# Optimization experiments

Hardware: AMD Instinct MI355X
Metric: run time of the kernel (lower is better)

## Reference

```python
import jax, jax.numpy as jnp
import numpy as np

B, T_RED, C = 16, 512, 512
MAX_DUR = 16


def setup_inputs() -> dict:
    key = jax.random.key(0)
    rng = np.random.default_rng(0)
    durs = np.zeros((B, T_RED), dtype=np.int32)
    for b in range(B):
        nv = int(rng.integers(T_RED // 2, T_RED + 1))
        durs[b, :nv] = rng.integers(1, MAX_DUR + 1, size=nv)
    target_T = durs.sum(axis=1).astype(np.int32)
    pooled_x = jax.random.normal(key, (B, T_RED, C), dtype=jnp.float32)
    return {
        "pooled_x": pooled_x,
        "durations": jnp.asarray(durs),
        "target_T": jnp.asarray(target_T),
    }


def reference(pooled_x, durations, target_T):
    # pooled_x: [B, T_red, C]; durations: [B, T_red] int (0 = pad); target_T: [B]
    Bv, T_red, Cv = pooled_x.shape
    max_len = int(jnp.max(target_T))  # concrete (eager) like the torch .item()

    # torch: valid_durs = durations[b][durations[b] > 0]; feats = pooled_x[b, :num_valid]
    # -> stably compact nonzero durations to the front; pair with leading features.
    order = jnp.argsort(jnp.where(durations > 0, 0, 1), axis=1, stable=True)
    d = jnp.take_along_axis(durations, order, axis=1)            # [B, T_red]
    csum = jnp.cumsum(d, axis=1)                                 # [B, T_red]

    t = jnp.arange(max_len, dtype=csum.dtype)                    # [max_len]
    # repeat_interleave inverse: output frame t belongs to segment
    # s = searchsorted(csum, t, 'right')  (csum[s-1] <= t < csum[s])
    seg = jax.vmap(lambda c: jnp.searchsorted(c, t, side="right"))(csum)  # [B, max_len]
    seg = jnp.minimum(seg, T_red - 1)

    total = csum[:, -1]                                          # len(repeat_interleave result)
    curr_len = jnp.minimum(total, target_T)                      # [B]
    valid = t[None, :] < curr_len[:, None]                       # [B, max_len]

    gathered = jnp.take_along_axis(pooled_x, seg[:, :, None], axis=1)  # [B, max_len, C]
    x_restored = jnp.where(valid[:, :, None], gathered, jnp.zeros((), pooled_x.dtype))
    new_mask = jnp.where(valid, 0, 1).astype(jnp.int32)          # 0 = valid, 1 = padded
    return x_restored, new_mask
```

## Files before the change

### kernel.cpp

```cpp
#include <hip/hip_runtime.h>
#include <hip/hip_bf16.h>

#define B_DIM 16
#define T_RED 512
#define C_DIM 512
#define ROWS_PER_BLK 16

typedef float vfloat4 __attribute__((ext_vector_type(4)));

__device__ inline int wave_incl_scan(int v) {
    #pragma unroll
    for (int off = 1; off < 64; off <<= 1) {
        int n = __shfl_up(v, off, 64);
        if ((threadIdx.x & 63) >= off) v += n;
    }
    return v;
}

__device__ inline int block_incl_scan(int v, int* wsum ) {
    const int lane = threadIdx.x & 63;
    const int wid  = threadIdx.x >> 6;
    int s = wave_incl_scan(v);
    if (lane == 63) wsum[wid] = s;
    __syncthreads();
    if (wid == 0 && lane < 8) {
        int w = wsum[lane];
        #pragma unroll
        for (int off = 1; off < 8; off <<= 1) {
            int n = __shfl_up(w, off, 8);
            if (lane >= off) w += n;
        }
        wsum[lane] = w;
    }
    __syncthreads();
    if (wid > 0) s += wsum[wid - 1];
    return s;
}

__global__ void build_rowmap(const int* __restrict__ durations,
                             int* __restrict__ rowsrc, int max_len) {
    const int b = blockIdx.x;
    const int tid = threadIdx.x;

    __shared__ int wsum[8];
    __shared__ int dcomp[T_RED];
    __shared__ int csum_s[T_RED];

    const int d = durations[b * T_RED + tid];
    const int f = (d > 0) ? 1 : 0;

    const int pos = block_incl_scan(f, wsum);
    dcomp[tid] = 0;
    __syncthreads();
    if (f) dcomp[pos - 1] = d;
    __syncthreads();

    const int myd = dcomp[tid];
    __syncthreads();
    const int cs = block_incl_scan(myd, wsum);
    csum_s[tid] = cs;
    __syncthreads();

    const int total = csum_s[T_RED - 1];
    const int start = cs - myd;
    const int srcrow = b * T_RED + tid;

    for (int k = 0; k < myd; ++k)
        rowsrc[b * max_len + start + k] = srcrow;

    for (int t = total + tid; t < max_len; t += T_RED)
        rowsrc[b * max_len + t] = -1;
}

__global__ __launch_bounds__(256) void scatter_rows(
        const vfloat4* __restrict__ x4,
        const int* __restrict__ rowsrc,
        vfloat4* __restrict__ out4,
        float* __restrict__ out_mask,
        int nrows) {
    __shared__ int ls[ROWS_PER_BLK];
    const int base = blockIdx.x * ROWS_PER_BLK;
    const int tid  = threadIdx.x;

    if (tid < ROWS_PER_BLK) {
        const int r = base + tid;
        const int s = (r < nrows) ? rowsrc[r] : -1;
        ls[tid] = s;
        if (r < nrows)
            __builtin_nontemporal_store((s >= 0) ? 0.0f : 1.0f, &out_mask[r]);
    }
    __syncthreads();

    const int c4   = tid & 127;
    const int half = tid >> 7;

    #pragma unroll
    for (int p = 0; p < 8; ++p) {
        const int lr = 2 * p + half;
        const int r  = base + lr;
        if (r < nrows) {
            const int s = ls[lr];
            vfloat4 v = (vfloat4)(0.0f);
            if (s >= 0) v = x4[(size_t)s * (C_DIM / 4) + c4];
            __builtin_nontemporal_store(v, &out4[(size_t)r * (C_DIM / 4) + c4]);
        }
    }
}

extern "C" void kernel_launch(void* const* d_in, const int* in_sizes, int n_in,
                              void* d_out, int out_size, void* d_ws, size_t ws_size,
                              hipStream_t stream) {
    const float* pooled_x  = (const float*)d_in[0];
    const int*   durations = (const int*)d_in[1];

    const int max_len = out_size / (B_DIM * (C_DIM + 1));
    const int nrows   = B_DIM * max_len;

    float* out_x    = (float*)d_out;
    float* out_mask = out_x + (size_t)nrows * C_DIM;

    int* rowsrc = (int*)d_ws;

    build_rowmap<<<B_DIM, T_RED, 0, stream>>>(durations, rowsrc, max_len);

    scatter_rows<<<(nrows + ROWS_PER_BLK - 1) / ROWS_PER_BLK, 256, 0, stream>>>(
        (const vfloat4*)pooled_x, rowsrc, (vfloat4*)out_x, out_mask, nrows);
}
```

Measured before the change: 161.7 us.

## Fuse row-map construction into scatter kernel with per-block scan and binary search

Removes the separate build_rowmap kernel and its global rowsrc buffer. Every scatter block now reloads its batch's durations, recomputes the compaction and cumulative sum in shared memory, and finds each output row's source segment by binary search. This drops one kernel launch and the serialized per-batch write loop, but repeats the scan work in every block. That adds several barriers before the copy phase starts.

```diff
diff --git a/kernel.cpp b/kernel.cpp
--- a/kernel.cpp
+++ b/kernel.cpp
@@ -8,101 +8,96 @@
 
 typedef float vfloat4 __attribute__((ext_vector_type(4)));
 
-__device__ inline int wave_incl_scan(int v) {
+__device__ inline int block_scan256(int v, int* wsum ) {
+    const int lane = threadIdx.x & 63;
+    const int wid  = threadIdx.x >> 6;
+    int s = v;
     #pragma unroll
     for (int off = 1; off < 64; off <<= 1) {
-        int n = __shfl_up(v, off, 64);
-        if ((threadIdx.x & 63) >= off) v += n;
+        int n = __shfl_up(s, off, 64);
+        if (lane >= off) s += n;
     }
-    return v;
+    if (lane == 63) wsum[wid] = s;
+    __syncthreads();
+    int add = 0;
+    #pragma unroll
+    for (int w = 0; w < 4; ++w)
+        if (w < wid) add += wsum[w];
+    int out = s + add;
+    __syncthreads();
+    return out;
 }
 
-__device__ inline int block_incl_scan(int v, int* wsum ) {
-    const int lane = threadIdx.x & 63;
-    const int wid  = threadIdx.x >> 6;
-    int s = wave_incl_scan(v);
-    if (lane == 63) wsum[wid] = s;
-    __syncthreads();
-    if (wid == 0 && lane < 8) {
-        int w = wsum[lane];
-        #pragma unroll
-        for (int off = 1; off < 8; off <<= 1) {
-            int n = __shfl_up(w, off, 8);
-            if (lane >= off) w += n;
-        }
-        wsum[lane] = w;
-    }
-    __syncthreads();
-    if (wid > 0) s += wsum[wid - 1];
-    return s;
-}
-
-__global__ void build_rowmap(const int* __restrict__ durations,
-                             int* __restrict__ rowsrc, int max_len) {
-    const int b = blockIdx.x;
-    const int tid = threadIdx.x;
-
-    __shared__ int wsum[8];
-    __shared__ int dcomp[T_RED];
-    __shared__ int csum_s[T_RED];
-
-    const int d = durations[b * T_RED + tid];
-    const int f = (d > 0) ? 1 : 0;
-
-    const int pos = block_incl_scan(f, wsum);
-    dcomp[tid] = 0;
-    __syncthreads();
-    if (f) dcomp[pos - 1] = d;
-    __syncthreads();
-
-    const int myd = dcomp[tid];
-    __syncthreads();
-    const int cs = block_incl_scan(myd, wsum);
-    csum_s[tid] = cs;
-    __syncthreads();
-
-    const int total = csum_s[T_RED - 1];
-    const int start = cs - myd;
-    const int srcrow = b * T_RED + tid;
-
-    for (int k = 0; k < myd; ++k)
-        rowsrc[b * max_len + start + k] = srcrow;
-
-    for (int t = total + tid; t < max_len; t += T_RED)
-        rowsrc[b * max_len + t] = -1;
-}
-
-__global__ __launch_bounds__(256) void scatter_rows(
+__global__ __launch_bounds__(256) void scatter_fused(
         const vfloat4* __restrict__ x4,
-        const int* __restrict__ rowsrc,
+        const int2* __restrict__ dur2,
         vfloat4* __restrict__ out4,
         float* __restrict__ out_mask,
-        int nrows) {
-    __shared__ int ls[ROWS_PER_BLK];
+        int max_len) {
+    const int b    = blockIdx.y;
     const int base = blockIdx.x * ROWS_PER_BLK;
     const int tid  = threadIdx.x;
 
+    __shared__ int dcomp[T_RED];
+    __shared__ int csum[T_RED];
+    __shared__ int wsum[4];
+    __shared__ int ls[ROWS_PER_BLK];
+
+    const int2 dd = dur2[b * (T_RED / 2) + tid];
+    const int d0 = dd.x, d1 = dd.y;
+    const int f0 = (d0 > 0) ? 1 : 0;
+    const int f1 = (d1 > 0) ? 1 : 0;
+
+    const int S1 = block_scan256(f0 + f1, wsum);
+    const int excl = S1 - f0 - f1;
+    dcomp[2 * tid]     = 0;
+    dcomp[2 * tid + 1] = 0;
+    __syncthreads();
+    if (f0) dcomp[excl] = d0;
+    if (f1) dcomp[excl + f0] = d1;
+    __syncthreads();
+
+    const int c0 = dcomp[2 * tid];
+    const int c1 = dcomp[2 * tid + 1];
+    const int S2 = block_scan256(c0 + c1, wsum);
+    csum[2 * tid]     = S2 - c1;
+    csum[2 * tid + 1] = S2;
+    __syncthreads();
+
+    const int total = csum[T_RED - 1];
+
     if (tid < ROWS_PER_BLK) {
-        const int r = base + tid;
-        const int s = (r < nrows) ? rowsrc[r] : -1;
-        ls[tid] = s;
-        if (r < nrows)
-            __builtin_nontemporal_store((s >= 0) ? 0.0f : 1.0f, &out_mask[r]);
+        const int t = base + tid;
+        int src = -1;
+        if (t < max_len && t < total) {
+            int idx = 0;
+            #pragma unroll
+            for (int w = 256; w >= 1; w >>= 1) {
+                const int cand = idx + w;
+                if (cand <= T_RED && csum[cand - 1] <= t) idx = cand;
+            }
+            const int seg = (idx < T_RED - 1) ? idx : (T_RED - 1);
+            src = b * T_RED + seg;
+        }
+        if (t < max_len) {
+            ls[tid] = src;
+            out_mask[(size_t)b * max_len + t] = (src >= 0) ? 0.0f : 1.0f;
+        }
     }
     __syncthreads();
 
     const int c4   = tid & 127;
     const int half = tid >> 7;
-
     #pragma unroll
     for (int p = 0; p < 8; ++p) {
         const int lr = 2 * p + half;
-        const int r  = base + lr;
-        if (r < nrows) {
+        const int t  = base + lr;
+        if (t < max_len) {
             const int s = ls[lr];
             vfloat4 v = (vfloat4)(0.0f);
             if (s >= 0) v = x4[(size_t)s * (C_DIM / 4) + c4];
-            __builtin_nontemporal_store(v, &out4[(size_t)r * (C_DIM / 4) + c4]);
+            __builtin_nontemporal_store(
+                v, &out4[((size_t)b * max_len + t) * (C_DIM / 4) + c4]);
         }
     }
 }
@@ -114,15 +109,12 @@
     const int*   durations = (const int*)d_in[1];
 
     const int max_len = out_size / (B_DIM * (C_DIM + 1));
-    const int nrows   = B_DIM * max_len;
 
     float* out_x    = (float*)d_out;
-    float* out_mask = out_x + (size_t)nrows * C_DIM;
+    float* out_mask = out_x + (size_t)B_DIM * max_len * C_DIM;
 
-    int* rowsrc = (int*)d_ws;
-
-    build_rowmap<<<B_DIM, T_RED, 0, stream>>>(durations, rowsrc, max_len);
-
-    scatter_rows<<<(nrows + ROWS_PER_BLK - 1) / ROWS_PER_BLK, 256, 0, stream>>>(
-        (const vfloat4*)pooled_x, rowsrc, (vfloat4*)out_x, out_mask, nrows);
+    dim3 grid((max_len + ROWS_PER_BLK - 1) / ROWS_PER_BLK, B_DIM);
+    scatter_fused<<<grid, 256, 0, stream>>>(
+        (const vfloat4*)pooled_x, (const int2*)durations,
+        (vfloat4*)out_x, out_mask, max_len);
 }
```

After: 160.4 us, median of 2. No clear change (-0.8%).
